# Kernel optimization log

Hardware: AMD Instinct MI355X
Metric: run time of the kernel (lower is better)

## Reference

```python
import jax, jax.numpy as jnp
import numpy as np

N_NODES = 100000
N_EDGES = 1200000
IN_CH = 128
HID = 64
EPS = 1e-5


def setup_inputs() -> dict:
    key = jax.random.key(0)
    ks = jax.random.split(key, 12)
    x = jax.random.normal(ks[0], (N_NODES, IN_CH), dtype=jnp.float32)
    edge_index = jax.random.randint(ks[1], (2, N_EDGES), 0, N_NODES, dtype=jnp.int64)
    def lin(k, i, o):
        s = 1.0 / np.sqrt(i)
        return jax.random.uniform(k, (i, o), jnp.float32, -s, s)
    return {
        "x": x,
        "edge_index": edge_index,
        "W1": lin(ks[2], IN_CH, HID), "b1": jnp.zeros((HID,), jnp.float32),
        "g1": jnp.ones((HID,), jnp.float32), "be1": jnp.zeros((HID,), jnp.float32),
        "W2": lin(ks[3], HID, HID), "b2": jnp.zeros((HID,), jnp.float32),
        "g2": jnp.ones((HID,), jnp.float32), "be2": jnp.zeros((HID,), jnp.float32),
        "Wm1": lin(ks[4], HID, HID // 2), "bm1": jnp.zeros((HID // 2,), jnp.float32),
        "Wm2": lin(ks[5], HID // 2, HID // 4), "bm2": jnp.zeros((HID // 4,), jnp.float32),
        "Wm3": lin(ks[6], HID // 4, 1), "bm3": jnp.zeros((1,), jnp.float32),
    }


def _gcn(x, edge_index, W, b, n_nodes):
    # GCNConv: out = D^-1/2 (A + I) D^-1/2 (x W) + b
    ar = jnp.arange(n_nodes, dtype=edge_index.dtype)
    src = jnp.concatenate([edge_index[0], ar])  # self-loops appended
    dst = jnp.concatenate([edge_index[1], ar])
    deg = jax.ops.segment_sum(jnp.ones_like(dst, dtype=x.dtype), dst,
                              num_segments=n_nodes)
    dinv = jax.lax.rsqrt(jnp.maximum(deg, 1.0))  # deg >= 1 due to self-loops
    norm = dinv[src] * dinv[dst]                 # [E+N]
    h = x @ W                                    # [N, out]
    msg = h[src] * norm[:, None]                 # gather (irregular)
    out = jax.ops.segment_sum(msg, dst, num_segments=n_nodes)  # scatter-add
    return out + b


def _bn(x, g, b):
    mu = jnp.mean(x, axis=0)
    var = jnp.mean(jnp.square(x - mu), axis=0)
    return (x - mu) * jax.lax.rsqrt(var + EPS) * g + b


def reference(x, edge_index, W1, b1, g1, be1, W2, b2, g2, be2,
              Wm1, bm1, Wm2, bm2, Wm3, bm3):
    n = x.shape[0]
    h = jax.nn.relu(_bn(_gcn(x, edge_index, W1, b1, n), g1, be1))
    h = jax.nn.relu(_bn(_gcn(h, edge_index, W2, b2, n), g2, be2))
    h = jax.nn.relu(h @ Wm1 + bm1)
    h = jax.nn.relu(h @ Wm2 + bm2)
    out = jax.nn.sigmoid(h @ Wm3 + bm3)
    return out.squeeze(-1)
```

## Files before the change

### kernel.cpp

```cpp
#include <hip/hip_runtime.h>
#include <hip/hip_fp16.h>
#include <math.h>

#define NN 100000
#define NE 1200000
#define INC 128
#define HIDC 64
#define EPSV 1e-5f
#define NPB 1024
#define NBUCK ((NN + NPB - 1) / NPB)
#define CAP 16384
#define CHUNK 8192

typedef float f4 __attribute__((ext_vector_type(4)));
typedef _Float16 hf;
typedef _Float16 h4 __attribute__((ext_vector_type(4)));
typedef _Float16 h8 __attribute__((ext_vector_type(8)));
typedef unsigned long long u64;

__global__ __launch_bounds__(256) void k_binit(
    int* bucketCur, float* stats,
    const float* __restrict__ W1, const float* __restrict__ W2,
    hf* __restrict__ w1t, hf* __restrict__ w2t) {
    int t = threadIdx.x;
    if (t < NBUCK) bucketCur[t] = t * CAP;
    if (t < 256) stats[t] = 0.f;
    for (int i = t; i < 64 * 128; i += 256) {
        int c = i >> 7, k = i & 127;
        w1t[i] = (hf)W1[k * 64 + c];
    }
    for (int i = t; i < 64 * 64; i += 256) {
        int c = i >> 6, k = i & 63;
        w2t[i] = (hf)W2[k * 64 + c];
    }
}

__global__ __launch_bounds__(256) void k_partA(
    const int* __restrict__ src, const int* __restrict__ dst,
    int* bucketCur, u64* __restrict__ pairs) {
    __shared__ int hist[NBUCK], base[NBUCK];
    int t = threadIdx.x;
    if (t < NBUCK) hist[t] = 0;
    __syncthreads();
    int e0 = blockIdx.x * CHUNK;
    int dloc[32];
#pragma unroll
    for (int j = 0; j < 32; ++j) {
        int e = e0 + j * 256 + t;
        int d = (e < NE) ? dst[e] : -1;
        dloc[j] = d;
        if (d >= 0) atomicAdd(&hist[d >> 10], 1);
    }
    __syncthreads();
    if (t < NBUCK) base[t] = hist[t] ? atomicAdd(&bucketCur[t], hist[t]) : 0;
    __syncthreads();
    if (t < NBUCK) hist[t] = 0;
    __syncthreads();
#pragma unroll
    for (int j = 0; j < 32; ++j) {
        int e = e0 + j * 256 + t;
        int d = dloc[j];
        if (d >= 0) {
            int b = d >> 10;
            int pos = base[b] + atomicAdd(&hist[b], 1);
            pairs[pos] = ((u64)(unsigned)d << 32) | (unsigned)src[e];
        }
    }
}

__global__ __launch_bounds__(256) void k_partB(
    const int* __restrict__ bucketCur, const u64* __restrict__ pairs,
    int* __restrict__ srcSorted, u64* __restrict__ cursPacked, float* __restrict__ dinv) {
    __shared__ int cnt1024[NPB];
    __shared__ int off1024[NPB];
    __shared__ int part[256];
    int b = blockIdx.x, t = threadIdx.x;
    int nbase = b * NPB;
    int beg = b * CAP;
    int end = bucketCur[b];
    for (int i = t; i < NPB; i += 256) cnt1024[i] = 0;
    __syncthreads();
    for (int i = beg + t; i < end; i += 256)
        atomicAdd(&cnt1024[(int)(pairs[i] >> 32) - nbase], 1);
    __syncthreads();
    int c[4]; int s = 0;
#pragma unroll
    for (int j = 0; j < 4; ++j) { c[j] = cnt1024[t * 4 + j]; s += c[j]; }
    part[t] = s;
    __syncthreads();
    for (int off = 1; off < 256; off <<= 1) {
        int x = (t >= off) ? part[t - off] : 0;
        __syncthreads();
        part[t] += x;
        __syncthreads();
    }
    int run = part[t] - s;
#pragma unroll
    for (int j = 0; j < 4; ++j) {
        int node = nbase + t * 4 + j;
        if (node < NN) {
            int nb = beg + run;
            cursPacked[node] = ((u64)(unsigned)(nb + c[j]) << 32) | (unsigned)nb;
            off1024[t * 4 + j] = run;
            dinv[node] = rsqrtf((float)c[j] + 1.0f);
            run += c[j];
        }
    }
    __syncthreads();
    for (int i = beg + t; i < end; i += 256) {
        u64 p = pairs[i];
        int d = (int)(p >> 32);
        int pos = beg + atomicAdd(&off1024[d - nbase], 1);
        srcSorted[pos] = (int)(p & 0xffffffffu);
    }
}

__global__ __launch_bounds__(256) void k_gemm1(
    const float* __restrict__ x, const hf* __restrict__ w1t,
    const float* __restrict__ dinv, hf* __restrict__ hp) {
    int wv = threadIdx.x >> 6, l = threadIdx.x & 63;
    int r16 = l & 15, kg = l >> 4;
    int nodeBase = blockIdx.x * 64;
    int row = nodeBase + wv * 16 + r16;
    int rowC = row < NN ? row : NN - 1;
    const float* xr = x + (size_t)rowC * INC + kg * 8;
    f4 acc[4] = {{0.f,0.f,0.f,0.f},{0.f,0.f,0.f,0.f},{0.f,0.f,0.f,0.f},{0.f,0.f,0.f,0.f}};
#pragma unroll
    for (int ks = 0; ks < 4; ++ks) {
        f4 alo = *(const f4*)(xr + ks * 32);
        f4 ahi = *(const f4*)(xr + ks * 32 + 4);
        h8 a;
#pragma unroll
        for (int j = 0; j < 4; ++j) { a[j] = (hf)alo[j]; a[4 + j] = (hf)ahi[j]; }
#pragma unroll
        for (int n = 0; n < 4; ++n) {
            h8 b = *(const h8*)(w1t + (n * 16 + r16) * INC + ks * 32 + kg * 8);
            acc[n] = __builtin_amdgcn_mfma_f32_16x16x32_f16(a, b, acc[n], 0, 0, 0);
        }
    }
#pragma unroll
    for (int j = 0; j < 4; ++j) {
        int nrow = nodeBase + wv * 16 + kg * 4 + j;
        if (nrow < NN) {
            float dv = dinv[nrow];
            size_t o = (size_t)nrow * HIDC + r16;
#pragma unroll
            for (int n = 0; n < 4; ++n)
                hp[o + n * 16] = (hf)(acc[n][j] * dv);
        }
    }
}

__global__ __launch_bounds__(256) void k_gemm2(
    const hf* __restrict__ agg, const hf* __restrict__ w2t,
    const float* __restrict__ scale, const float* __restrict__ shift,
    const float* __restrict__ dinv, hf* __restrict__ hp) {
    int wv = threadIdx.x >> 6, l = threadIdx.x & 63;
    int r16 = l & 15, kg = l >> 4;
    int nodeBase = blockIdx.x * 64;
    int row = nodeBase + wv * 16 + r16;
    int rowC = row < NN ? row : NN - 1;
    const hf* ar = agg + (size_t)rowC * HIDC + kg * 8;
    f4 acc[4] = {{0.f,0.f,0.f,0.f},{0.f,0.f,0.f,0.f},{0.f,0.f,0.f,0.f},{0.f,0.f,0.f,0.f}};
#pragma unroll
    for (int ks = 0; ks < 2; ++ks) {
        h8 raw = *(const h8*)(ar + ks * 32);
        int ch0 = ks * 32 + kg * 8;
        h8 a;
#pragma unroll
        for (int j = 0; j < 8; ++j) {
            float v = (float)raw[j] * scale[ch0 + j] + shift[ch0 + j];
            a[j] = (hf)fmaxf(v, 0.f);
        }
#pragma unroll
        for (int n = 0; n < 4; ++n) {
            h8 b = *(const h8*)(w2t + (n * 16 + r16) * HIDC + ks * 32 + kg * 8);
            acc[n] = __builtin_amdgcn_mfma_f32_16x16x32_f16(a, b, acc[n], 0, 0, 0);
        }
    }
#pragma unroll
    for (int j = 0; j < 4; ++j) {
        int nrow = nodeBase + wv * 16 + kg * 4 + j;
        if (nrow < NN) {
            float dv = dinv[nrow];
            size_t o = (size_t)nrow * HIDC + r16;
#pragma unroll
            for (int n = 0; n < 4; ++n)
                hp[o + n * 16] = (hf)(acc[n][j] * dv);
        }
    }
}

__global__ __launch_bounds__(256) void k_gather(
    const u64* __restrict__ cursPacked, const int* __restrict__ srcSorted,
    const float* __restrict__ dinv, const hf* __restrict__ hp,
    hf* __restrict__ agg) {
    int wid = threadIdx.x >> 6, lane = threadIdx.x & 63;
    int n = blockIdx.x * 4 + wid;
    if (n >= NN) return;
    u64 ce = cursPacked[n];
    int beg = (int)(ce & 0xffffffffu);
    int end = (int)(ce >> 32);
    float acc = (float)hp[(size_t)n * HIDC + lane];
    for (int base = beg; base < end; base += 64) {
        int m = end - base; if (m > 64) m = 64;
        int si = (base + lane < end) ? srcSorted[base + lane] : 0;
        int j = 0;
        for (; j + 8 <= m; j += 8) {
            int s0 = __shfl(si, j),     s1 = __shfl(si, j + 1);
            int s2 = __shfl(si, j + 2), s3 = __shfl(si, j + 3);
            int s4 = __shfl(si, j + 4), s5 = __shfl(si, j + 5);
            int s6 = __shfl(si, j + 6), s7 = __shfl(si, j + 7);
            float v0 = (float)hp[(size_t)s0 * HIDC + lane];
            float v1 = (float)hp[(size_t)s1 * HIDC + lane];
            float v2 = (float)hp[(size_t)s2 * HIDC + lane];
            float v3 = (float)hp[(size_t)s3 * HIDC + lane];
            float v4 = (float)hp[(size_t)s4 * HIDC + lane];
            float v5 = (float)hp[(size_t)s5 * HIDC + lane];
            float v6 = (float)hp[(size_t)s6 * HIDC + lane];
            float v7 = (float)hp[(size_t)s7 * HIDC + lane];
            acc += ((v0 + v1) + (v2 + v3)) + ((v4 + v5) + (v6 + v7));
        }
        for (; j + 2 <= m; j += 2) {
            int s0 = __shfl(si, j), s1 = __shfl(si, j + 1);
            float v0 = (float)hp[(size_t)s0 * HIDC + lane];
            float v1 = (float)hp[(size_t)s1 * HIDC + lane];
            acc += v0 + v1;
        }
        if (j < m) {
            int s = __shfl(si, j);
            acc += (float)hp[(size_t)s * HIDC + lane];
        }
    }
    agg[(size_t)n * HIDC + lane] = (hf)(dinv[n] * acc);
}

__global__ __launch_bounds__(256) void k_stats(
    const hf* __restrict__ agg, float* gsum, float* gsq) {
    __shared__ float ls[256], lq[256];
    int tid = threadIdx.x;
    int c = tid & 63, r = tid >> 6;
    float s = 0.0f, q = 0.0f;
    for (int n = blockIdx.x * 4 + r; n < NN; n += gridDim.x * 4) {
        float v = (float)agg[(size_t)n * HIDC + c];
        s += v; q += v * v;
    }
    ls[tid] = s; lq[tid] = q;
    __syncthreads();
    if (tid < 64) {
        s = ls[tid] + ls[tid + 64] + ls[tid + 128] + ls[tid + 192];
        q = lq[tid] + lq[tid + 64] + lq[tid + 128] + lq[tid + 192];
        atomicAdd(&gsum[c], s);
        atomicAdd(&gsq[c], q);
    }
}

__global__ void k_bnfin(const float* __restrict__ gsum, const float* __restrict__ gsq,
                        const float* __restrict__ g, const float* __restrict__ be,
                        float* scale, float* shift) {
    int c = threadIdx.x;
    if (c < HIDC) {
        float mu = gsum[c] * (1.0f / NN);
        float var = gsq[c] * (1.0f / NN) - mu * mu;
        float inv = rsqrtf(var + EPSV);
        float sc = g[c] * inv;
        scale[c] = sc;
        shift[c] = be[c] - mu * sc;
    }
}

__global__ __launch_bounds__(256) void k_mlp(
    const hf* __restrict__ agg, const float* __restrict__ scale,
    const float* __restrict__ shift,
    const float* __restrict__ Wm1, const float* __restrict__ bm1,
    const float* __restrict__ Wm2, const float* __restrict__ bm2,
    const float* __restrict__ Wm3, const float* __restrict__ bm3,
    float* __restrict__ out) {
    int n = blockIdx.x * blockDim.x + threadIdx.x;
    if (n >= NN) return;
    float h[HIDC];
#pragma unroll
    for (int cq = 0; cq < 8; ++cq) {
        h8 v8 = *(const h8*)&agg[(size_t)n * HIDC + cq * 8];
#pragma unroll
        for (int j = 0; j < 8; ++j) {
            int c = cq * 8 + j;
            h[c] = fmaxf((float)v8[j] * scale[c] + shift[c], 0.0f);
        }
    }
    float a1[32];
#pragma unroll
    for (int j = 0; j < 32; ++j) {
        float acc = bm1[j];
#pragma unroll
        for (int c = 0; c < HIDC; ++c) acc += h[c] * Wm1[c * 32 + j];
        a1[j] = fmaxf(acc, 0.0f);
    }
    float a2[16];
#pragma unroll
    for (int j = 0; j < 16; ++j) {
        float acc = bm2[j];
#pragma unroll
        for (int c = 0; c < 32; ++c) acc += a1[c] * Wm2[c * 16 + j];
        a2[j] = fmaxf(acc, 0.0f);
    }
    float z = bm3[0];
#pragma unroll
    for (int c = 0; c < 16; ++c) z += a2[c] * Wm3[c];
    out[n] = 1.0f / (1.0f + expf(-z));
}

extern "C" void kernel_launch(void* const* d_in, const int* in_sizes, int n_in,
                              void* d_out, int out_size, void* d_ws, size_t ws_size,
                              hipStream_t stream) {
    const float* x   = (const float*)d_in[0];
    const int*   ei  = (const int*)d_in[1];
    const float* W1  = (const float*)d_in[2];
    const float* g1  = (const float*)d_in[4];
    const float* be1 = (const float*)d_in[5];
    const float* W2  = (const float*)d_in[6];
    const float* g2  = (const float*)d_in[8];
    const float* be2 = (const float*)d_in[9];
    const float* Wm1 = (const float*)d_in[10];
    const float* bm1 = (const float*)d_in[11];
    const float* Wm2 = (const float*)d_in[12];
    const float* bm2 = (const float*)d_in[13];
    const float* Wm3 = (const float*)d_in[14];
    const float* bm3 = (const float*)d_in[15];
    float* out = (float*)d_out;

    const int* srcI = ei;
    const int* dstI = ei + NE;

    const size_t CAPT = (size_t)NBUCK * CAP;
    int*   bucketCur = (int*)d_ws;
    float* stats     = (float*)(bucketCur + 128);
    u64*   cursPacked= (u64*)(stats + 512);
    int*   srcSorted = (int*)(cursPacked + NN);
    float* dinv      = (float*)(srcSorted + CAPT);
    hf*    w1t       = (hf*)(dinv + NN);
    hf*    w2t       = w1t + 64 * 128;
    hf*    hp        = w2t + 64 * 64;
    hf*    agg       = hp + (size_t)NN * HIDC;
    u64*   pairs     = (u64*)(agg + (size_t)NN * HIDC);
    float *sum1 = stats,       *sq1 = stats + 64;
    float *sum2 = stats + 128, *sq2 = stats + 192;
    float *scale1 = stats + 256, *shift1 = stats + 320;
    float *scale2 = stats + 384, *shift2 = stats + 448;

    k_binit<<<1, 256, 0, stream>>>(bucketCur, stats, W1, W2, w1t, w2t);
    k_partA<<<(NE + CHUNK - 1) / CHUNK, 256, 0, stream>>>(srcI, dstI, bucketCur, pairs);
    k_partB<<<NBUCK, 256, 0, stream>>>(bucketCur, pairs, srcSorted, cursPacked, dinv);

    k_gemm1<<<(NN + 63) / 64, 256, 0, stream>>>(x, w1t, dinv, hp);
    k_gather<<<(NN + 3) / 4, 256, 0, stream>>>(cursPacked, srcSorted, dinv, hp, agg);
    k_stats<<<512, 256, 0, stream>>>(agg, sum1, sq1);
    k_bnfin<<<1, 64, 0, stream>>>(sum1, sq1, g1, be1, scale1, shift1);

    k_gemm2<<<(NN + 63) / 64, 256, 0, stream>>>(agg, w2t, scale1, shift1, dinv, hp);
    k_gather<<<(NN + 3) / 4, 256, 0, stream>>>(cursPacked, srcSorted, dinv, hp, agg);
    k_stats<<<512, 256, 0, stream>>>(agg, sum2, sq2);
    k_bnfin<<<1, 64, 0, stream>>>(sum2, sq2, g2, be2, scale2, shift2);

    k_mlp<<<(NN + 255) / 256, 256, 0, stream>>>(agg, scale2, shift2,
                                                Wm1, bm1, Wm2, bm2, Wm3, bm3, out);
}
```

Before: 266.1 us.

## Pad per-node neighbor lists to 16 with zero row; pack pairs into 32 bits

Pads each node's CSR neighbor segment to a multiple of 16 with a sentinel index pointing at an extra all-zero row of hp. This lets the gather loop process neighbors in fixed blocks of 16 with two accumulators and no remainder handling. The partition pairs are also packed into 32 bits (local destination plus source index) instead of 64 bits, which halves the pair traffic in the bucketing kernels. The cost is extra wasted loads of the zero row (about 7.5 per node on average) and a larger srcSorted buffer that needs sentinel fill. The 17-bit source field relies on the node count staying below 131072.

```diff
diff --git a/kernel.cpp b/kernel.cpp
--- a/kernel.cpp
+++ b/kernel.cpp
@@ -9,22 +9,24 @@
 #define EPSV 1e-5f
 #define NPB 1024
 #define NBUCK ((NN + NPB - 1) / NPB)
-#define CAP 16384
+#define PCAP 16384
+#define SCAP 24576
 #define CHUNK 8192
 
 typedef float f4 __attribute__((ext_vector_type(4)));
 typedef _Float16 hf;
-typedef _Float16 h4 __attribute__((ext_vector_type(4)));
 typedef _Float16 h8 __attribute__((ext_vector_type(8)));
+typedef unsigned int u32;
 typedef unsigned long long u64;
 
 __global__ __launch_bounds__(256) void k_binit(
     int* bucketCur, float* stats,
     const float* __restrict__ W1, const float* __restrict__ W2,
-    hf* __restrict__ w1t, hf* __restrict__ w2t) {
+    hf* __restrict__ w1t, hf* __restrict__ w2t, hf* __restrict__ hp) {
     int t = threadIdx.x;
-    if (t < NBUCK) bucketCur[t] = t * CAP;
+    if (t < NBUCK) bucketCur[t] = t * PCAP;
     if (t < 256) stats[t] = 0.f;
+    if (t < HIDC) hp[(size_t)NN * HIDC + t] = (hf)0.f;
     for (int i = t; i < 64 * 128; i += 256) {
         int c = i >> 7, k = i & 127;
         w1t[i] = (hf)W1[k * 64 + c];
@@ -37,7 +39,7 @@
 
 __global__ __launch_bounds__(256) void k_partA(
     const int* __restrict__ src, const int* __restrict__ dst,
-    int* bucketCur, u64* __restrict__ pairs) {
+    int* bucketCur, u32* __restrict__ pairs) {
     __shared__ int hist[NBUCK], base[NBUCK];
     int t = threadIdx.x;
     if (t < NBUCK) hist[t] = 0;
@@ -63,29 +65,35 @@
         if (d >= 0) {
             int b = d >> 10;
             int pos = base[b] + atomicAdd(&hist[b], 1);
-            pairs[pos] = ((u64)(unsigned)d << 32) | (unsigned)src[e];
+            pairs[pos] = ((u32)(d & 1023) << 17) | (u32)src[e];
         }
     }
 }
 
 __global__ __launch_bounds__(256) void k_partB(
-    const int* __restrict__ bucketCur, const u64* __restrict__ pairs,
+    const int* __restrict__ bucketCur, const u32* __restrict__ pairs,
     int* __restrict__ srcSorted, u64* __restrict__ cursPacked, float* __restrict__ dinv) {
     __shared__ int cnt1024[NPB];
     __shared__ int off1024[NPB];
     __shared__ int part[256];
+    __shared__ int totPad;
     int b = blockIdx.x, t = threadIdx.x;
     int nbase = b * NPB;
-    int beg = b * CAP;
-    int end = bucketCur[b];
+    int pbeg = b * PCAP;
+    int pend = bucketCur[b];
+    int sbeg = b * SCAP;
     for (int i = t; i < NPB; i += 256) cnt1024[i] = 0;
     __syncthreads();
-    for (int i = beg + t; i < end; i += 256)
-        atomicAdd(&cnt1024[(int)(pairs[i] >> 32) - nbase], 1);
-    __syncthreads();
-    int c[4]; int s = 0;
-#pragma unroll
-    for (int j = 0; j < 4; ++j) { c[j] = cnt1024[t * 4 + j]; s += c[j]; }
+    for (int i = pbeg + t; i < pend; i += 256)
+        atomicAdd(&cnt1024[pairs[i] >> 17], 1);
+    __syncthreads();
+    int c[4], pc[4]; int s = 0;
+#pragma unroll
+    for (int j = 0; j < 4; ++j) {
+        c[j] = cnt1024[t * 4 + j];
+        pc[j] = (c[j] + 15) & ~15;
+        s += pc[j];
+    }
     part[t] = s;
     __syncthreads();
     for (int off = 1; off < 256; off <<= 1) {
@@ -94,24 +102,28 @@
         part[t] += x;
         __syncthreads();
     }
+    if (t == 255) totPad = part[255];
     int run = part[t] - s;
 #pragma unroll
     for (int j = 0; j < 4; ++j) {
         int node = nbase + t * 4 + j;
         if (node < NN) {
-            int nb = beg + run;
-            cursPacked[node] = ((u64)(unsigned)(nb + c[j]) << 32) | (unsigned)nb;
+            int nb = sbeg + run;
+            cursPacked[node] = ((u64)(u32)(nb + pc[j]) << 32) | (u32)nb;
             off1024[t * 4 + j] = run;
             dinv[node] = rsqrtf((float)c[j] + 1.0f);
-            run += c[j];
-        }
-    }
-    __syncthreads();
-    for (int i = beg + t; i < end; i += 256) {
-        u64 p = pairs[i];
-        int d = (int)(p >> 32);
-        int pos = beg + atomicAdd(&off1024[d - nbase], 1);
-        srcSorted[pos] = (int)(p & 0xffffffffu);
+            run += pc[j];
+        }
+    }
+    __syncthreads();
+    int tp = totPad;
+    for (int i = t; i < tp; i += 256) srcSorted[sbeg + i] = NN;
+    __syncthreads();
+    for (int i = pbeg + t; i < pend; i += 256) {
+        u32 p = pairs[i];
+        int dl = (int)(p >> 17);
+        int pos = sbeg + atomicAdd(&off1024[dl], 1);
+        srcSorted[pos] = (int)(p & 0x1FFFFu);
     }
 }
 
@@ -201,38 +213,41 @@
     u64 ce = cursPacked[n];
     int beg = (int)(ce & 0xffffffffu);
     int end = (int)(ce >> 32);
-    float acc = (float)hp[(size_t)n * HIDC + lane];
+    float accA = (float)hp[(size_t)n * HIDC + lane];
+    float accB = 0.f;
     for (int base = beg; base < end; base += 64) {
         int m = end - base; if (m > 64) m = 64;
         int si = (base + lane < end) ? srcSorted[base + lane] : 0;
-        int j = 0;
-        for (; j + 8 <= m; j += 8) {
-            int s0 = __shfl(si, j),     s1 = __shfl(si, j + 1);
-            int s2 = __shfl(si, j + 2), s3 = __shfl(si, j + 3);
-            int s4 = __shfl(si, j + 4), s5 = __shfl(si, j + 5);
-            int s6 = __shfl(si, j + 6), s7 = __shfl(si, j + 7);
-            float v0 = (float)hp[(size_t)s0 * HIDC + lane];
-            float v1 = (float)hp[(size_t)s1 * HIDC + lane];
-            float v2 = (float)hp[(size_t)s2 * HIDC + lane];
-            float v3 = (float)hp[(size_t)s3 * HIDC + lane];
-            float v4 = (float)hp[(size_t)s4 * HIDC + lane];
-            float v5 = (float)hp[(size_t)s5 * HIDC + lane];
-            float v6 = (float)hp[(size_t)s6 * HIDC + lane];
-            float v7 = (float)hp[(size_t)s7 * HIDC + lane];
-            acc += ((v0 + v1) + (v2 + v3)) + ((v4 + v5) + (v6 + v7));
-        }
-        for (; j + 2 <= m; j += 2) {
-            int s0 = __shfl(si, j), s1 = __shfl(si, j + 1);
-            float v0 = (float)hp[(size_t)s0 * HIDC + lane];
-            float v1 = (float)hp[(size_t)s1 * HIDC + lane];
-            acc += v0 + v1;
-        }
-        if (j < m) {
-            int s = __shfl(si, j);
-            acc += (float)hp[(size_t)s * HIDC + lane];
-        }
-    }
-    agg[(size_t)n * HIDC + lane] = (hf)(dinv[n] * acc);
+        for (int j = 0; j < m; j += 16) {
+            int s0  = __shfl(si, j),      s1  = __shfl(si, j + 1);
+            int s2  = __shfl(si, j + 2),  s3  = __shfl(si, j + 3);
+            int s4  = __shfl(si, j + 4),  s5  = __shfl(si, j + 5);
+            int s6  = __shfl(si, j + 6),  s7  = __shfl(si, j + 7);
+            int s8  = __shfl(si, j + 8),  s9  = __shfl(si, j + 9);
+            int s10 = __shfl(si, j + 10), s11 = __shfl(si, j + 11);
+            int s12 = __shfl(si, j + 12), s13 = __shfl(si, j + 13);
+            int s14 = __shfl(si, j + 14), s15 = __shfl(si, j + 15);
+            float v0  = (float)hp[(size_t)s0  * HIDC + lane];
+            float v1  = (float)hp[(size_t)s1  * HIDC + lane];
+            float v2  = (float)hp[(size_t)s2  * HIDC + lane];
+            float v3  = (float)hp[(size_t)s3  * HIDC + lane];
+            float v4  = (float)hp[(size_t)s4  * HIDC + lane];
+            float v5  = (float)hp[(size_t)s5  * HIDC + lane];
+            float v6  = (float)hp[(size_t)s6  * HIDC + lane];
+            float v7  = (float)hp[(size_t)s7  * HIDC + lane];
+            float v8  = (float)hp[(size_t)s8  * HIDC + lane];
+            float v9  = (float)hp[(size_t)s9  * HIDC + lane];
+            float v10 = (float)hp[(size_t)s10 * HIDC + lane];
+            float v11 = (float)hp[(size_t)s11 * HIDC + lane];
+            float v12 = (float)hp[(size_t)s12 * HIDC + lane];
+            float v13 = (float)hp[(size_t)s13 * HIDC + lane];
+            float v14 = (float)hp[(size_t)s14 * HIDC + lane];
+            float v15 = (float)hp[(size_t)s15 * HIDC + lane];
+            accA += (((v0 + v1) + (v2 + v3)) + ((v4 + v5) + (v6 + v7)));
+            accB += (((v8 + v9) + (v10 + v11)) + ((v12 + v13) + (v14 + v15)));
+        }
+    }
+    agg[(size_t)n * HIDC + lane] = (hf)(dinv[n] * (accA + accB));
 }
 
 __global__ __launch_bounds__(256) void k_stats(
@@ -332,23 +347,24 @@
     const int* srcI = ei;
     const int* dstI = ei + NE;
 
-    const size_t CAPT = (size_t)NBUCK * CAP;
+    const size_t PCAPT = (size_t)NBUCK * PCAP;
+    const size_t SCAPT = (size_t)NBUCK * SCAP;
     int*   bucketCur = (int*)d_ws;
     float* stats     = (float*)(bucketCur + 128);
     u64*   cursPacked= (u64*)(stats + 512);
     int*   srcSorted = (int*)(cursPacked + NN);
-    float* dinv      = (float*)(srcSorted + CAPT);
+    float* dinv      = (float*)(srcSorted + SCAPT);
     hf*    w1t       = (hf*)(dinv + NN);
     hf*    w2t       = w1t + 64 * 128;
     hf*    hp        = w2t + 64 * 64;
-    hf*    agg       = hp + (size_t)NN * HIDC;
-    u64*   pairs     = (u64*)(agg + (size_t)NN * HIDC);
+    hf*    agg       = hp + (size_t)(NN + 1) * HIDC;
+    u32*   pairs     = (u32*)(agg + (size_t)NN * HIDC);
     float *sum1 = stats,       *sq1 = stats + 64;
     float *sum2 = stats + 128, *sq2 = stats + 192;
     float *scale1 = stats + 256, *shift1 = stats + 320;
     float *scale2 = stats + 384, *shift2 = stats + 448;
 
-    k_binit<<<1, 256, 0, stream>>>(bucketCur, stats, W1, W2, w1t, w2t);
+    k_binit<<<1, 256, 0, stream>>>(bucketCur, stats, W1, W2, w1t, w2t, hp);
     k_partA<<<(NE + CHUNK - 1) / CHUNK, 256, 0, stream>>>(srcI, dstI, bucketCur, pairs);
     k_partB<<<NBUCK, 256, 0, stream>>>(bucketCur, pairs, srcSorted, cursPacked, dinv);
 
```

Result: faster. 253.7 us (-4.7%).
